# Kernel tuning notes

Measured on AMD Instinct MI355X. Metric: run time of the kernel, lower is better.

## Reference

```python
import jax, jax.numpy as jnp
import numpy as np

N, DEG, IN_DIM, HID, OUT = 50000, 32, 256, 256, 128

def setup_inputs() -> dict:
    key = jax.random.key(0)
    k1, k2, k3, k4, k5, k6 = jax.random.split(key, 6)
    node_features = jax.random.normal(k1, (N, IN_DIM), dtype=jnp.float32)
    neighbor_idx = jax.random.randint(k2, (N, DEG), 0, N)
    scale1 = 1.0 / np.sqrt(2 * IN_DIM)
    scale2 = 1.0 / np.sqrt(HID)
    W1 = jax.random.normal(k3, (HID, 2 * IN_DIM), dtype=jnp.float32) * scale1
    b1 = jax.random.normal(k4, (HID,), dtype=jnp.float32) * scale1
    W2 = jax.random.normal(k5, (OUT, HID), dtype=jnp.float32) * scale2
    b2 = jax.random.normal(k6, (OUT,), dtype=jnp.float32) * scale2
    return {"node_features": node_features, "neighbor_idx": neighbor_idx,
            "W1": W1, "b1": b1, "W2": W2, "b2": b2}

def reference(node_features, neighbor_idx, W1, b1, W2, b2):
    # Layer 0 (mean aggregator, with neighbors):
    # gather [N, DEG, IN_DIM] neighbor features, mean over DEG
    nbr_mean = jnp.mean(node_features[neighbor_idx], axis=1)  # [N, IN_DIM]
    combined = jnp.concatenate([node_features, nbr_mean], axis=-1)  # [N, 2*IN_DIM]
    h = jax.nn.relu(combined @ W1.T + b1)  # [N, HID]
    # Layer 1: empty neighbor list -> linear_without_neighbors + relu
    out = jax.nn.relu(h @ W2.T + b2)  # [N, OUT]
    return out
```

## Files before the change

kernel.cpp:

```cpp
#include <hip/hip_runtime.h>
#include <stdint.h>

#define N_NODES 50000
#define DEG     32
#define IN_DIM  256
#define K1      512
#define HID     256
#define OUT_DIM 128

#define NCHUNK  4
#define CDIM    64
#define SLICE8  ((size_t)N_NODES * CDIM)
#define GT      16

#define MT   64
#define CSTR 520
#define HSTR 264

typedef __bf16 bf16x8 __attribute__((ext_vector_type(8)));
typedef float  f32x4  __attribute__((ext_vector_type(4)));
typedef float  f32x2  __attribute__((ext_vector_type(2)));

__device__ __forceinline__ unsigned short f2bf(float f) {
    union { float f; unsigned u; } v; v.f = f;
    unsigned r = v.u + 0x7fffu + ((v.u >> 16) & 1u);
    return (unsigned short)(r >> 16);
}
__device__ __forceinline__ int clampN(int v) {
    return v < 0 ? 0 : (v >= N_NODES ? N_NODES - 1 : v);
}

__global__ __launch_bounds__(256)
void cvt_feat(const float* __restrict__ feat,
              unsigned short* __restrict__ featb,
              unsigned char*  __restrict__ featF8)
{
    const int t    = threadIdx.x;
    const int node = blockIdx.x * 8 + (t >> 5);
    const int seg  = t & 31;
    if (node < N_NODES) {
        const float4* src = (const float4*)(feat + (size_t)node * IN_DIM + seg * 8);
        float4 f0 = src[0], f1 = src[1];
        ushort4 o0, o1;
        o0.x = f2bf(f0.x); o0.y = f2bf(f0.y); o0.z = f2bf(f0.z); o0.w = f2bf(f0.w);
        o1.x = f2bf(f1.x); o1.y = f2bf(f1.y); o1.z = f2bf(f1.z); o1.w = f2bf(f1.w);
        unsigned short* db = featb + (size_t)node * IN_DIM + seg * 8;
        *(ushort4*)db       = o0;
        *(ushort4*)(db + 4) = o1;
        int u0 = 0, u1 = 0;
        u0 = __builtin_amdgcn_cvt_pk_fp8_f32(f0.x, f0.y, u0, false);
        u0 = __builtin_amdgcn_cvt_pk_fp8_f32(f0.z, f0.w, u0, true);
        u1 = __builtin_amdgcn_cvt_pk_fp8_f32(f1.x, f1.y, u1, false);
        u1 = __builtin_amdgcn_cvt_pk_fp8_f32(f1.z, f1.w, u1, true);
        const int c   = seg >> 3;
        const int off = (seg & 7) * 8;
        unsigned char* d8 = featF8 + (size_t)c * SLICE8 + (size_t)node * CDIM + off;
        ((int*)d8)[0] = u0;
        ((int*)d8)[1] = u1;
    }
}

__global__ __launch_bounds__(256)
void prep_small(const float* __restrict__ W1, const float* __restrict__ W2,
                const int* __restrict__ nbr,
                unsigned short* __restrict__ W1b, unsigned short* __restrict__ W2b,
                unsigned short* __restrict__ nbr16) {
    const int stride = gridDim.x * blockDim.x * 4;
    const int tid4 = (blockIdx.x * blockDim.x + threadIdx.x) * 4;
    for (int i = tid4; i < HID * K1; i += stride) {
        float4 f = *(const float4*)(W1 + i);
        ushort4 o; o.x = f2bf(f.x); o.y = f2bf(f.y); o.z = f2bf(f.z); o.w = f2bf(f.w);
        *(ushort4*)(W1b + i) = o;
    }
    for (int i = tid4; i < OUT_DIM * HID; i += stride) {
        float4 f = *(const float4*)(W2 + i);
        ushort4 o; o.x = f2bf(f.x); o.y = f2bf(f.y); o.z = f2bf(f.z); o.w = f2bf(f.w);
        *(ushort4*)(W2b + i) = o;
    }
    for (int i = tid4; i < N_NODES * DEG; i += stride) {
        int4 v = *(const int4*)(nbr + i);
        ushort4 o;
        o.x = (unsigned short)clampN(v.x); o.y = (unsigned short)clampN(v.y);
        o.z = (unsigned short)clampN(v.z); o.w = (unsigned short)clampN(v.w);
        *(ushort4*)(nbr16 + i) = o;
    }
}

__global__ __launch_bounds__(256)
void gather_mean_fp8(const unsigned char*  __restrict__ featF8,
                     const unsigned short* __restrict__ nbr16,
                     unsigned short*       __restrict__ meanb)
{
    __shared__ unsigned short sIdx[GT * DEG];
    const int tid  = threadIdx.x;
    const int c    = blockIdx.y;
    const int base = blockIdx.x * GT;

    if (tid < 128) {
        *(ushort4*)(sIdx + tid * 4) =
            *(const ushort4*)(nbr16 + (size_t)base * DEG + tid * 4);
    }
    __syncthreads();

    const unsigned char* slice = featF8 + (size_t)c * SLICE8;
    const int grp = tid >> 4;
    const int ln  = tid & 15;
    const unsigned short* idxr = sIdx + grp * DEG;

    float s0 = 0.f, s1 = 0.f, s2 = 0.f, s3 = 0.f;
    #pragma unroll 8
    for (int j = 0; j < DEG; ++j) {
        int nb = idxr[j];
        unsigned v = *(const unsigned*)(slice + (size_t)nb * CDIM + ln * 4);
        f32x2 lo = __builtin_amdgcn_cvt_pk_f32_fp8(v, false);
        f32x2 hi = __builtin_amdgcn_cvt_pk_f32_fp8(v, true);
        s0 += lo[0]; s1 += lo[1]; s2 += hi[0]; s3 += hi[1];
    }
    const float sc = 1.0f / 32.0f;
    ushort4 o;
    o.x = f2bf(s0 * sc); o.y = f2bf(s1 * sc);
    o.z = f2bf(s2 * sc); o.w = f2bf(s3 * sc);
    const int node = base + grp;
    *(ushort4*)(meanb + (size_t)node * IN_DIM + c * CDIM + ln * 4) = o;
}

__global__ __launch_bounds__(512, 4)
void sage_gemm(const unsigned short* __restrict__ featb,
               const unsigned short* __restrict__ meanb,
               const unsigned short* __restrict__ W1b,
               const float*          __restrict__ b1,
               const unsigned short* __restrict__ W2b,
               const float*          __restrict__ b2,
               float*                __restrict__ out)
{
    __shared__ __align__(16) unsigned short sBuf[MT * CSTR];
    unsigned short* sC = sBuf;
    unsigned short* sH = sBuf;

    const int tid  = threadIdx.x;
    const int lane = tid & 63;
    const int wave = tid >> 6;
    const int base = blockIdx.x * MT;

    for (int i = wave * 8; i < wave * 8 + 8; ++i) {
        const int node = base + i;
        if (node < N_NODES) {
            const unsigned short* src = (lane < 32)
                ? featb + (size_t)node * IN_DIM + lane * 8
                : meanb + (size_t)node * IN_DIM + (lane - 32) * 8;
            *(bf16x8*)(&sC[i * CSTR + lane * 8]) = *(const bf16x8*)src;
        } else {
            bf16x8 z = (bf16x8){0, 0, 0, 0, 0, 0, 0, 0};
            *(bf16x8*)(&sC[i * CSTR + lane * 8]) = z;
        }
    }
    __syncthreads();

    const int r = lane & 15;
    const int q = lane >> 4;

    {
        f32x4 acc[4][2];
        #pragma unroll
        for (int mt = 0; mt < 4; ++mt)
            #pragma unroll
            for (int nt = 0; nt < 2; ++nt)
                acc[mt][nt] = (f32x4){0.f, 0.f, 0.f, 0.f};

        for (int k0 = 0; k0 < K1; k0 += 32) {
            bf16x8 a[4];
            #pragma unroll
            for (int mt = 0; mt < 4; ++mt)
                a[mt] = *(const bf16x8*)(&sC[(mt * 16 + r) * CSTR + k0 + q * 8]);
            #pragma unroll
            for (int nt = 0; nt < 2; ++nt) {
                int n = wave * 32 + nt * 16 + r;
                bf16x8 b = *(const bf16x8*)(W1b + (size_t)n * K1 + k0 + q * 8);
                #pragma unroll
                for (int mt = 0; mt < 4; ++mt)
                    acc[mt][nt] = __builtin_amdgcn_mfma_f32_16x16x32_bf16(a[mt], b, acc[mt][nt], 0, 0, 0);
            }
        }
        __syncthreads();
        #pragma unroll
        for (int nt = 0; nt < 2; ++nt) {
            int n = wave * 32 + nt * 16 + r;
            float bias = b1[n];
            #pragma unroll
            for (int mt = 0; mt < 4; ++mt)
                #pragma unroll
                for (int g = 0; g < 4; ++g) {
                    int m = mt * 16 + q * 4 + g;
                    float v = acc[mt][nt][g] + bias;
                    sH[m * HSTR + n] = f2bf(v > 0.f ? v : 0.f);
                }
        }
    }
    __syncthreads();

    {
        f32x4 acc[4];
        #pragma unroll
        for (int mt = 0; mt < 4; ++mt) acc[mt] = (f32x4){0.f, 0.f, 0.f, 0.f};

        const int o = wave * 16 + r;
        for (int k0 = 0; k0 < HID; k0 += 32) {
            bf16x8 b = *(const bf16x8*)(W2b + (size_t)o * HID + k0 + q * 8);
            #pragma unroll
            for (int mt = 0; mt < 4; ++mt) {
                bf16x8 a = *(const bf16x8*)(&sH[(mt * 16 + r) * HSTR + k0 + q * 8]);
                acc[mt] = __builtin_amdgcn_mfma_f32_16x16x32_bf16(a, b, acc[mt], 0, 0, 0);
            }
        }
        float bias = b2[o];
        #pragma unroll
        for (int mt = 0; mt < 4; ++mt)
            #pragma unroll
            for (int g = 0; g < 4; ++g) {
                int m = mt * 16 + q * 4 + g;
                int node = base + m;
                if (node < N_NODES) {
                    float v = acc[mt][g] + bias;
                    out[(size_t)node * OUT_DIM + o] = v > 0.f ? v : 0.f;
                }
            }
    }
}

__global__ __launch_bounds__(256)
void sage_naive(const float* __restrict__ feat, const int* __restrict__ nbr,
                const float* __restrict__ W1, const float* __restrict__ b1,
                const float* __restrict__ W2, const float* __restrict__ b2,
                float* __restrict__ out) {
    __shared__ float comb[K1];
    __shared__ float h[HID];
    const int node = blockIdx.x;
    const int t = threadIdx.x;
    comb[t] = feat[(size_t)node * IN_DIM + t];
    float acc = 0.f;
    for (int d = 0; d < DEG; ++d) {
        int nb = clampN(nbr[node * DEG + d]);
        acc += feat[(size_t)nb * IN_DIM + t];
    }
    comb[IN_DIM + t] = acc * (1.0f / 32.0f);
    __syncthreads();
    float s = b1[t];
    for (int k = 0; k < K1; ++k) s += comb[k] * W1[(size_t)t * K1 + k];
    h[t] = s > 0.f ? s : 0.f;
    __syncthreads();
    if (t < OUT_DIM) {
        float s2 = b2[t];
        for (int k = 0; k < HID; ++k) s2 += h[k] * W2[(size_t)t * HID + k];
        out[(size_t)node * OUT_DIM + t] = s2 > 0.f ? s2 : 0.f;
    }
}

extern "C" void kernel_launch(void* const* d_in, const int* in_sizes, int n_in,
                              void* d_out, int out_size, void* d_ws, size_t ws_size,
                              hipStream_t stream) {
    const float* feat = (const float*)d_in[0];
    const int*   nbr  = (const int*)d_in[1];
    const float* W1   = (const float*)d_in[2];
    const float* b1   = (const float*)d_in[3];
    const float* W2   = (const float*)d_in[4];
    const float* b2   = (const float*)d_in[5];
    float* out = (float*)d_out;

    const size_t feat_elems = (size_t)N_NODES * IN_DIM;
    const size_t w1_elems   = (size_t)HID * K1;
    const size_t w2_elems   = (size_t)OUT_DIM * HID;
    const size_t mean_elems = (size_t)N_NODES * IN_DIM;
    const size_t idx_elems  = (size_t)N_NODES * DEG;
    const size_t u16_elems  = feat_elems + w1_elems + w2_elems + mean_elems + idx_elems;
    const size_t need = u16_elems * sizeof(unsigned short)
                      + (size_t)NCHUNK * SLICE8;

    if (ws_size >= need) {
        unsigned short* featb  = (unsigned short*)d_ws;
        unsigned short* W1b    = featb + feat_elems;
        unsigned short* W2b    = W1b + w1_elems;
        unsigned short* meanb  = W2b + w2_elems;
        unsigned short* nbr16  = meanb + mean_elems;
        unsigned char*  featF8 = (unsigned char*)(nbr16 + idx_elems);

        cvt_feat<<<(N_NODES + 7) / 8, 256, 0, stream>>>(feat, featb, featF8);
        prep_small<<<256, 256, 0, stream>>>(W1, W2, nbr, W1b, W2b, nbr16);
        gather_mean_fp8<<<dim3(N_NODES / GT, NCHUNK), 256, 0, stream>>>(featF8, nbr16, meanb);
        sage_gemm<<<(N_NODES + MT - 1) / MT, 512, 0, stream>>>(featb, meanb, W1b, b1, W2b, b2, out);
    } else {
        sage_naive<<<N_NODES, 256, 0, stream>>>(feat, nbr, W1, b1, W2, b2, out);
    }
}
```

Before: 194.9 us.

## Make the GEMM persistent with register-resident weights and merge the prep kernels

The fused two-layer GEMM becomes a persistent kernel with 256 blocks that loop over 64-node tiles. Each wave loads its slices of W1 and W2 and the biases into registers once, instead of reloading the weight fragments from global memory for every tile. The two prep kernels (feature conversion and weight/index conversion) are merged into one launch to save a launch. In exchange, the weight fragments need a large register budget that the launch bounds may not allow, which risks spills. The kernel also runs fewer waves per CU, and tile loads are no longer overlapped with compute across blocks.

```diff
diff --git a/kernel.cpp b/kernel.cpp
--- a/kernel.cpp
+++ b/kernel.cpp
@@ -13,9 +13,11 @@
 #define SLICE8  ((size_t)N_NODES * CDIM)
 #define GT      16
 
-#define MT   64
-#define CSTR 520
-#define HSTR 264
+#define MT     64
+#define NTILES 782
+#define GBLK   256
+#define CSTR   520
+#define HSTR   264
 
 typedef __bf16 bf16x8 __attribute__((ext_vector_type(8)));
 typedef float  f32x4  __attribute__((ext_vector_type(4)));
@@ -30,59 +32,61 @@
     return v < 0 ? 0 : (v >= N_NODES ? N_NODES - 1 : v);
 }
 
+#define FEAT_BLKS ((N_NODES + 7) / 8)
 __global__ __launch_bounds__(256)
-void cvt_feat(const float* __restrict__ feat,
+void prep_all(const float* __restrict__ feat,
+              const float* __restrict__ W1, const float* __restrict__ W2,
+              const int*   __restrict__ nbr,
               unsigned short* __restrict__ featb,
-              unsigned char*  __restrict__ featF8)
+              unsigned char*  __restrict__ featF8,
+              unsigned short* __restrict__ W1b, unsigned short* __restrict__ W2b,
+              unsigned short* __restrict__ nbr16)
 {
-    const int t    = threadIdx.x;
-    const int node = blockIdx.x * 8 + (t >> 5);
-    const int seg  = t & 31;
-    if (node < N_NODES) {
-        const float4* src = (const float4*)(feat + (size_t)node * IN_DIM + seg * 8);
-        float4 f0 = src[0], f1 = src[1];
-        ushort4 o0, o1;
-        o0.x = f2bf(f0.x); o0.y = f2bf(f0.y); o0.z = f2bf(f0.z); o0.w = f2bf(f0.w);
-        o1.x = f2bf(f1.x); o1.y = f2bf(f1.y); o1.z = f2bf(f1.z); o1.w = f2bf(f1.w);
-        unsigned short* db = featb + (size_t)node * IN_DIM + seg * 8;
-        *(ushort4*)db       = o0;
-        *(ushort4*)(db + 4) = o1;
-        int u0 = 0, u1 = 0;
-        u0 = __builtin_amdgcn_cvt_pk_fp8_f32(f0.x, f0.y, u0, false);
-        u0 = __builtin_amdgcn_cvt_pk_fp8_f32(f0.z, f0.w, u0, true);
-        u1 = __builtin_amdgcn_cvt_pk_fp8_f32(f1.x, f1.y, u1, false);
-        u1 = __builtin_amdgcn_cvt_pk_fp8_f32(f1.z, f1.w, u1, true);
-        const int c   = seg >> 3;
-        const int off = (seg & 7) * 8;
-        unsigned char* d8 = featF8 + (size_t)c * SLICE8 + (size_t)node * CDIM + off;
-        ((int*)d8)[0] = u0;
-        ((int*)d8)[1] = u1;
-    }
-}
-
-__global__ __launch_bounds__(256)
-void prep_small(const float* __restrict__ W1, const float* __restrict__ W2,
-                const int* __restrict__ nbr,
-                unsigned short* __restrict__ W1b, unsigned short* __restrict__ W2b,
-                unsigned short* __restrict__ nbr16) {
-    const int stride = gridDim.x * blockDim.x * 4;
-    const int tid4 = (blockIdx.x * blockDim.x + threadIdx.x) * 4;
-    for (int i = tid4; i < HID * K1; i += stride) {
-        float4 f = *(const float4*)(W1 + i);
-        ushort4 o; o.x = f2bf(f.x); o.y = f2bf(f.y); o.z = f2bf(f.z); o.w = f2bf(f.w);
-        *(ushort4*)(W1b + i) = o;
-    }
-    for (int i = tid4; i < OUT_DIM * HID; i += stride) {
-        float4 f = *(const float4*)(W2 + i);
-        ushort4 o; o.x = f2bf(f.x); o.y = f2bf(f.y); o.z = f2bf(f.z); o.w = f2bf(f.w);
-        *(ushort4*)(W2b + i) = o;
-    }
-    for (int i = tid4; i < N_NODES * DEG; i += stride) {
-        int4 v = *(const int4*)(nbr + i);
-        ushort4 o;
-        o.x = (unsigned short)clampN(v.x); o.y = (unsigned short)clampN(v.y);
-        o.z = (unsigned short)clampN(v.z); o.w = (unsigned short)clampN(v.w);
-        *(ushort4*)(nbr16 + i) = o;
+    const int t = threadIdx.x;
+    if (blockIdx.x < FEAT_BLKS) {
+        const int node = blockIdx.x * 8 + (t >> 5);
+        const int seg  = t & 31;
+        if (node < N_NODES) {
+            const float4* src = (const float4*)(feat + (size_t)node * IN_DIM + seg * 8);
+            float4 f0 = src[0], f1 = src[1];
+            ushort4 o0, o1;
+            o0.x = f2bf(f0.x); o0.y = f2bf(f0.y); o0.z = f2bf(f0.z); o0.w = f2bf(f0.w);
+            o1.x = f2bf(f1.x); o1.y = f2bf(f1.y); o1.z = f2bf(f1.z); o1.w = f2bf(f1.w);
+            unsigned short* db = featb + (size_t)node * IN_DIM + seg * 8;
+            *(ushort4*)db       = o0;
+            *(ushort4*)(db + 4) = o1;
+            int u0 = 0, u1 = 0;
+            u0 = __builtin_amdgcn_cvt_pk_fp8_f32(f0.x, f0.y, u0, false);
+            u0 = __builtin_amdgcn_cvt_pk_fp8_f32(f0.z, f0.w, u0, true);
+            u1 = __builtin_amdgcn_cvt_pk_fp8_f32(f1.x, f1.y, u1, false);
+            u1 = __builtin_amdgcn_cvt_pk_fp8_f32(f1.z, f1.w, u1, true);
+            const int c   = seg >> 3;
+            const int off = (seg & 7) * 8;
+            unsigned char* d8 = featF8 + (size_t)c * SLICE8 + (size_t)node * CDIM + off;
+            ((int*)d8)[0] = u0;
+            ((int*)d8)[1] = u1;
+        }
+    } else {
+        const int bid = blockIdx.x - FEAT_BLKS;
+        const int stride = 256 * 256 * 4;
+        const int tid4 = (bid * 256 + t) * 4;
+        for (int i = tid4; i < HID * K1; i += stride) {
+            float4 f = *(const float4*)(W1 + i);
+            ushort4 o; o.x = f2bf(f.x); o.y = f2bf(f.y); o.z = f2bf(f.z); o.w = f2bf(f.w);
+            *(ushort4*)(W1b + i) = o;
+        }
+        for (int i = tid4; i < OUT_DIM * HID; i += stride) {
+            float4 f = *(const float4*)(W2 + i);
+            ushort4 o; o.x = f2bf(f.x); o.y = f2bf(f.y); o.z = f2bf(f.z); o.w = f2bf(f.w);
+            *(ushort4*)(W2b + i) = o;
+        }
+        for (int i = tid4; i < N_NODES * DEG; i += stride) {
+            int4 v = *(const int4*)(nbr + i);
+            ushort4 o;
+            o.x = (unsigned short)clampN(v.x); o.y = (unsigned short)clampN(v.y);
+            o.z = (unsigned short)clampN(v.z); o.w = (unsigned short)clampN(v.w);
+            *(ushort4*)(nbr16 + i) = o;
+        }
     }
 }
 
@@ -124,106 +128,122 @@
     *(ushort4*)(meanb + (size_t)node * IN_DIM + c * CDIM + ln * 4) = o;
 }
 
-__global__ __launch_bounds__(512, 4)
-void sage_gemm(const unsigned short* __restrict__ featb,
-               const unsigned short* __restrict__ meanb,
-               const unsigned short* __restrict__ W1b,
-               const float*          __restrict__ b1,
-               const unsigned short* __restrict__ W2b,
-               const float*          __restrict__ b2,
-               float*                __restrict__ out)
+__global__ __launch_bounds__(512, 2)
+void sage_gemm_reg(const unsigned short* __restrict__ featb,
+                   const unsigned short* __restrict__ meanb,
+                   const unsigned short* __restrict__ W1b,
+                   const float*          __restrict__ b1,
+                   const unsigned short* __restrict__ W2b,
+                   const float*          __restrict__ b2,
+                   float*                __restrict__ out)
 {
-    __shared__ __align__(16) unsigned short sBuf[MT * CSTR];
-    unsigned short* sC = sBuf;
-    unsigned short* sH = sBuf;
+    __shared__ __align__(16) unsigned short sC[MT * CSTR];
+    __shared__ __align__(16) unsigned short sH[MT * HSTR];
 
     const int tid  = threadIdx.x;
     const int lane = tid & 63;
     const int wave = tid >> 6;
-    const int base = blockIdx.x * MT;
-
-    for (int i = wave * 8; i < wave * 8 + 8; ++i) {
-        const int node = base + i;
-        if (node < N_NODES) {
-            const unsigned short* src = (lane < 32)
-                ? featb + (size_t)node * IN_DIM + lane * 8
-                : meanb + (size_t)node * IN_DIM + (lane - 32) * 8;
-            *(bf16x8*)(&sC[i * CSTR + lane * 8]) = *(const bf16x8*)src;
-        } else {
-            bf16x8 z = (bf16x8){0, 0, 0, 0, 0, 0, 0, 0};
-            *(bf16x8*)(&sC[i * CSTR + lane * 8]) = z;
-        }
-    }
-    __syncthreads();
-
-    const int r = lane & 15;
-    const int q = lane >> 4;
-
+    const int r    = lane & 15;
+    const int q    = lane >> 4;
+
+    bf16x8 w1f[2][16];
+    #pragma unroll
+    for (int nt = 0; nt < 2; ++nt) {
+        const size_t nrow = (size_t)(wave * 32 + nt * 16 + r) * K1;
+        #pragma unroll
+        for (int kk = 0; kk < 16; ++kk)
+            w1f[nt][kk] = *(const bf16x8*)(W1b + nrow + kk * 32 + q * 8);
+    }
+    bf16x8 w2f[8];
     {
-        f32x4 acc[4][2];
+        const size_t orow = (size_t)(wave * 16 + r) * HID;
         #pragma unroll
-        for (int mt = 0; mt < 4; ++mt)
-            #pragma unroll
-            for (int nt = 0; nt < 2; ++nt)
-                acc[mt][nt] = (f32x4){0.f, 0.f, 0.f, 0.f};
-
-        for (int k0 = 0; k0 < K1; k0 += 32) {
-            bf16x8 a[4];
+        for (int kk = 0; kk < 8; ++kk)
+            w2f[kk] = *(const bf16x8*)(W2b + orow + kk * 32 + q * 8);
+    }
+    const float bias1a = b1[wave * 32 + r];
+    const float bias1b = b1[wave * 32 + 16 + r];
+    const float bias2  = b2[wave * 16 + r];
+
+    for (int tile = blockIdx.x; tile < NTILES; tile += GBLK) {
+        const int base = tile * MT;
+
+        for (int i = wave * 8; i < wave * 8 + 8; ++i) {
+            const int node = base + i;
+            if (node < N_NODES) {
+                const unsigned short* src = (lane < 32)
+                    ? featb + (size_t)node * IN_DIM + lane * 8
+                    : meanb + (size_t)node * IN_DIM + (lane - 32) * 8;
+                *(bf16x8*)(&sC[i * CSTR + lane * 8]) = *(const bf16x8*)src;
+            } else {
+                bf16x8 z = (bf16x8){0, 0, 0, 0, 0, 0, 0, 0};
+                *(bf16x8*)(&sC[i * CSTR + lane * 8]) = z;
+            }
+        }
+        __syncthreads();
+
+        {
+            f32x4 acc[4][2];
             #pragma unroll
             for (int mt = 0; mt < 4; ++mt)
-                a[mt] = *(const bf16x8*)(&sC[(mt * 16 + r) * CSTR + k0 + q * 8]);
+                #pragma unroll
+                for (int nt = 0; nt < 2; ++nt)
+                    acc[mt][nt] = (f32x4){0.f, 0.f, 0.f, 0.f};
+
+            #pragma unroll
+            for (int kk = 0; kk < 16; ++kk) {
+                bf16x8 a[4];
+                #pragma unroll
+                for (int mt = 0; mt < 4; ++mt)
+                    a[mt] = *(const bf16x8*)(&sC[(mt * 16 + r) * CSTR + kk * 32 + q * 8]);
+                #pragma unroll
+                for (int nt = 0; nt < 2; ++nt)
+                    #pragma unroll
+                    for (int mt = 0; mt < 4; ++mt)
+                        acc[mt][nt] = __builtin_amdgcn_mfma_f32_16x16x32_bf16(a[mt], w1f[nt][kk], acc[mt][nt], 0, 0, 0);
+            }
             #pragma unroll
             for (int nt = 0; nt < 2; ++nt) {
-                int n = wave * 32 + nt * 16 + r;
-                bf16x8 b = *(const bf16x8*)(W1b + (size_t)n * K1 + k0 + q * 8);
+                const int n = wave * 32 + nt * 16 + r;
+                const float bias = nt ? bias1b : bias1a;
                 #pragma unroll
                 for (int mt = 0; mt < 4; ++mt)
-                    acc[mt][nt] = __builtin_amdgcn_mfma_f32_16x16x32_bf16(a[mt], b, acc[mt][nt], 0, 0, 0);
+                    #pragma unroll
+                    for (int g = 0; g < 4; ++g) {
+                        const int m = mt * 16 + q * 4 + g;
+                        float v = acc[mt][nt][g] + bias;
+                        sH[m * HSTR + n] = f2bf(v > 0.f ? v : 0.f);
+                    }
             }
         }
         __syncthreads();
-        #pragma unroll
-        for (int nt = 0; nt < 2; ++nt) {
-            int n = wave * 32 + nt * 16 + r;
-            float bias = b1[n];
+
+        {
+            f32x4 acc3[4];
+            #pragma unroll
+            for (int mt = 0; mt < 4; ++mt) acc3[mt] = (f32x4){0.f, 0.f, 0.f, 0.f};
+
+            #pragma unroll
+            for (int kk = 0; kk < 8; ++kk)
+                #pragma unroll
+                for (int mt = 0; mt < 4; ++mt) {
+                    bf16x8 a = *(const bf16x8*)(&sH[(mt * 16 + r) * HSTR + kk * 32 + q * 8]);
+                    acc3[mt] = __builtin_amdgcn_mfma_f32_16x16x32_bf16(a, w2f[kk], acc3[mt], 0, 0, 0);
+                }
+
+            const int o = wave * 16 + r;
             #pragma unroll
             for (int mt = 0; mt < 4; ++mt)
                 #pragma unroll
                 for (int g = 0; g < 4; ++g) {
-                    int m = mt * 16 + q * 4 + g;
-                    float v = acc[mt][nt][g] + bias;
-                    sH[m * HSTR + n] = f2bf(v > 0.f ? v : 0.f);
+                    const int m = mt * 16 + q * 4 + g;
+                    const int node = base + m;
+                    if (node < N_NODES) {
+                        float v = acc3[mt][g] + bias2;
+                        out[(size_t)node * OUT_DIM + o] = v > 0.f ? v : 0.f;
+                    }
                 }
         }
-    }
-    __syncthreads();
-
-    {
-        f32x4 acc[4];
-        #pragma unroll
-        for (int mt = 0; mt < 4; ++mt) acc[mt] = (f32x4){0.f, 0.f, 0.f, 0.f};
-
-        const int o = wave * 16 + r;
-        for (int k0 = 0; k0 < HID; k0 += 32) {
-            bf16x8 b = *(const bf16x8*)(W2b + (size_t)o * HID + k0 + q * 8);
-            #pragma unroll
-            for (int mt = 0; mt < 4; ++mt) {
-                bf16x8 a = *(const bf16x8*)(&sH[(mt * 16 + r) * HSTR + k0 + q * 8]);
-                acc[mt] = __builtin_amdgcn_mfma_f32_16x16x32_bf16(a, b, acc[mt], 0, 0, 0);
-            }
-        }
-        float bias = b2[o];
-        #pragma unroll
-        for (int mt = 0; mt < 4; ++mt)
-            #pragma unroll
-            for (int g = 0; g < 4; ++g) {
-                int m = mt * 16 + q * 4 + g;
-                int node = base + m;
-                if (node < N_NODES) {
-                    float v = acc[mt][g] + bias;
-                    out[(size_t)node * OUT_DIM + o] = v > 0.f ? v : 0.f;
-                }
-            }
     }
 }
 
@@ -283,10 +303,10 @@
         unsigned short* nbr16  = meanb + mean_elems;
         unsigned char*  featF8 = (unsigned char*)(nbr16 + idx_elems);
 
-        cvt_feat<<<(N_NODES + 7) / 8, 256, 0, stream>>>(feat, featb, featF8);
-        prep_small<<<256, 256, 0, stream>>>(W1, W2, nbr, W1b, W2b, nbr16);
+        prep_all<<<FEAT_BLKS + 256, 256, 0, stream>>>(feat, W1, W2, nbr,
+                                                      featb, featF8, W1b, W2b, nbr16);
         gather_mean_fp8<<<dim3(N_NODES / GT, NCHUNK), 256, 0, stream>>>(featF8, nbr16, meanb);
-        sage_gemm<<<(N_NODES + MT - 1) / MT, 512, 0, stream>>>(featb, meanb, W1b, b1, W2b, b2, out);
+        sage_gemm_reg<<<GBLK, 512, 0, stream>>>(featb, meanb, W1b, b1, W2b, b2, out);
     } else {
         sage_naive<<<N_NODES, 256, 0, stream>>>(feat, nbr, W1, b1, W2, b2, out);
     }
```

New measurement: 187.1 us. 1.04x faster.
